# Optimization experiments

Hardware: AMD Instinct MI355X
Metric: run time of the kernel (lower is better)

The kernel has to match this reference:

```python
import jax, jax.numpy as jnp
import numpy as np

D_MODEL = 1024
D_STATE = 16
D_CONV = 4
EXPAND = 2
D_INNER = EXPAND * D_MODEL
DT_RANK = (D_MODEL + 15) // 16  # ceil(d_model/16) = 64
BATCH, SEQ = 4, 4096


def setup_inputs() -> dict:
    key = jax.random.key(0)
    ks = jax.random.split(key, 8)
    s = 0.02
    x = jax.random.normal(ks[0], (BATCH, SEQ, D_MODEL), jnp.float32)
    in_proj_w = jax.random.normal(ks[1], (2 * D_INNER, D_MODEL), jnp.float32) * s
    conv_w = jax.random.normal(ks[2], (D_INNER, D_CONV), jnp.float32) * 0.2  # depthwise kernel
    conv_b = jnp.zeros((D_INNER,), jnp.float32)
    x_proj_w = jax.random.normal(ks[3], (DT_RANK + 2 * D_STATE, D_INNER), jnp.float32) * s
    dt_proj_w = jax.random.normal(ks[4], (D_INNER, DT_RANK), jnp.float32) * s
    # standard mamba dt bias init: softplus(bias) ~ small positive dt
    dt_proj_b = jnp.log(jnp.expm1(jnp.full((D_INNER,), 1e-2, jnp.float32)))
    # S4D-real init: A = -[1..d_state] per channel
    A_log = jnp.log(jnp.tile(jnp.arange(1, D_STATE + 1, dtype=jnp.float32), (D_INNER, 1)))
    D_skip = jnp.ones((D_INNER,), jnp.float32)
    out_proj_w = jax.random.normal(ks[5], (D_MODEL, D_INNER), jnp.float32) * s
    return dict(x=x, in_proj_w=in_proj_w, conv_w=conv_w, conv_b=conv_b,
                x_proj_w=x_proj_w, dt_proj_w=dt_proj_w, dt_proj_b=dt_proj_b,
                A_log=A_log, D_skip=D_skip, out_proj_w=out_proj_w)


def _rmsnorm(x, eps=1e-6):
    # FastSimpleRMSNorm: no learned weight
    return x * jax.lax.rsqrt(jnp.mean(x * x, axis=-1, keepdims=True) + eps)


def reference(x, in_proj_w, conv_w, conv_b, x_proj_w, dt_proj_w, dt_proj_b,
              A_log, D_skip, out_proj_w):
    B_, L, _ = x.shape
    u = _rmsnorm(x)
    # in_proj -> gate z and conv branch xc, each [B, L, d_inner]
    xz = jnp.einsum('bld,ed->ble', u, in_proj_w)
    xc, z = jnp.split(xz, 2, axis=-1)
    # causal depthwise conv1d (width D_CONV) + silu
    xp = jnp.pad(xc, ((0, 0), (D_CONV - 1, 0), (0, 0)))
    conv = conv_b + sum(conv_w[:, k] * xp[:, k:k + L, :] for k in range(D_CONV))
    xc = jax.nn.silu(conv)
    # x_proj -> dt, B, C
    dbl = jnp.einsum('ble,fe->blf', xc, x_proj_w)
    dt, Bm, Cm = jnp.split(dbl, [DT_RANK, DT_RANK + D_STATE], axis=-1)
    dt = jax.nn.softplus(jnp.einsum('blr,er->ble', dt, dt_proj_w) + dt_proj_b)  # [B,L,d_inner]
    A = -jnp.exp(A_log)  # [d_inner, d_state]

    def step(h, inp):
        dt_t, B_t, C_t, x_t = inp  # [B,d_inner],[B,d_state],[B,d_state],[B,d_inner]
        dA = jnp.exp(dt_t[..., None] * A)             # [B,d_inner,d_state]
        h = h * dA + (dt_t * x_t)[..., None] * B_t[:, None, :]
        y = jnp.einsum('bes,bs->be', h, C_t)
        return h, y

    h0 = jnp.zeros((B_, D_INNER, D_STATE), xc.dtype)
    xs = (jnp.swapaxes(dt, 0, 1), jnp.swapaxes(Bm, 0, 1),
          jnp.swapaxes(Cm, 0, 1), jnp.swapaxes(xc, 0, 1))
    _, ys = jax.lax.scan(step, h0, xs)                # [L,B,d_inner]
    y = jnp.swapaxes(ys, 0, 1) + D_skip * xc
    y = y * jax.nn.silu(z)
    out = jnp.einsum('ble,de->bld', y, out_proj_w)
    return x + out
```

## Files before the change

### kernel.cpp

```cpp
#include <hip/hip_runtime.h>
#include <hip/hip_bf16.h>
#include <math.h>

typedef __hip_bfloat16 bf16;
typedef __attribute__((ext_vector_type(8))) short short8;
typedef __attribute__((ext_vector_type(4))) float f32x4;

#define BATCH_N 4
#define SEQ_N 4096
#define DMODEL 1024
#define DINNER 2048
#define DTRANK 64
#define DSTATE 16
#define NROWS (BATCH_N * SEQ_N)

__device__ __forceinline__ float b2f(bf16 v) { return __bfloat162float(v); }
__device__ __forceinline__ bf16 f2b(float v) { return __float2bfloat16(v); }

__device__ __forceinline__ void gll16(const bf16* g, bf16* l) {
    __builtin_amdgcn_global_load_lds((const __attribute__((address_space(1))) unsigned int*)g,
                                     (__attribute__((address_space(3))) unsigned int*)l,
                                     16, 0, 0);
}

#define CVT_N1 4194304
#define CVT_N2 196608
#define CVT_N3 131072
#define CVT_N4 2097152
#define CVT_TOTAL (CVT_N1 + CVT_N2 + CVT_N3 + CVT_N4)
__global__ __launch_bounds__(256) void prep_kernel(const float* __restrict__ x, bf16* __restrict__ u,
                                                   const float* __restrict__ i1, bf16* __restrict__ o1,
                                                   const float* __restrict__ i2, bf16* __restrict__ o2,
                                                   const float* __restrict__ i3, bf16* __restrict__ o3,
                                                   const float* __restrict__ i4, bf16* __restrict__ o4) {
    if (blockIdx.x < NROWS) {
        const int r = blockIdx.x;
        const int t = threadIdx.x;
        const float4 v = reinterpret_cast<const float4*>(x + (size_t)r * DMODEL)[t];
        float ss = v.x * v.x + v.y * v.y + v.z * v.z + v.w * v.w;
        #pragma unroll
        for (int o = 32; o > 0; o >>= 1) ss += __shfl_down(ss, o);
        __shared__ float red[4];
        if ((t & 63) == 0) red[t >> 6] = ss;
        __syncthreads();
        const float tot = red[0] + red[1] + red[2] + red[3];
        const float rs = rsqrtf(tot * (1.0f / DMODEL) + 1e-6f);
        union { uint2 u2; bf16 h[4]; } o4v;
        o4v.h[0] = f2b(v.x * rs); o4v.h[1] = f2b(v.y * rs);
        o4v.h[2] = f2b(v.z * rs); o4v.h[3] = f2b(v.w * rs);
        *reinterpret_cast<uint2*>(u + (size_t)r * DMODEL + t * 4) = o4v.u2;
    } else {
        int i = (blockIdx.x - NROWS) * 256 + threadIdx.x;
        if (i < CVT_N1) { o1[i] = f2b(i1[i]); }
        i -= CVT_N1;
        if (i >= 0 && i < CVT_N2) { o2[i] = f2b(i2[i]); }
        i -= CVT_N2;
        if (i >= 0 && i < CVT_N3) { o3[i] = f2b(i3[i]); }
        i -= CVT_N3;
        if (i >= 0 && i < CVT_N4) { o4[i] = f2b(i4[i]); }
    }
}

__global__ __launch_bounds__(256) void conv_silu4_kernel(const bf16* __restrict__ xcraw,
                                                         const float* __restrict__ cw,
                                                         const float* __restrict__ cb,
                                                         bf16* __restrict__ xc) {
    const int t = blockIdx.x * 256 + threadIdx.x;
    const int e = (t << 2) & (DINNER - 1);
    const int r = t >> 9;
    const int l = r & (SEQ_N - 1);
    float4 w0 = *reinterpret_cast<const float4*>(cw + (e + 0) * 4);
    float4 w1 = *reinterpret_cast<const float4*>(cw + (e + 1) * 4);
    float4 w2 = *reinterpret_cast<const float4*>(cw + (e + 2) * 4);
    float4 w3 = *reinterpret_cast<const float4*>(cw + (e + 3) * 4);
    const float4 bias = *reinterpret_cast<const float4*>(cb + e);
    float xs[4][4];
    #pragma unroll
    for (int k = 0; k < 4; ++k) {
        const int lp = l - 3 + k;
        if (lp >= 0) {
            union { uint2 u; bf16 h[4]; } tmp;
            tmp.u = *reinterpret_cast<const uint2*>(xcraw + (size_t)(r - 3 + k) * DINNER + e);
            #pragma unroll
            for (int j = 0; j < 4; ++j) xs[k][j] = b2f(tmp.h[j]);
        } else {
            #pragma unroll
            for (int j = 0; j < 4; ++j) xs[k][j] = 0.f;
        }
    }
    float acc[4];
    acc[0] = bias.x + w0.x * xs[0][0] + w0.y * xs[1][0] + w0.z * xs[2][0] + w0.w * xs[3][0];
    acc[1] = bias.y + w1.x * xs[0][1] + w1.y * xs[1][1] + w1.z * xs[2][1] + w1.w * xs[3][1];
    acc[2] = bias.z + w2.x * xs[0][2] + w2.y * xs[1][2] + w2.z * xs[2][2] + w2.w * xs[3][2];
    acc[3] = bias.w + w3.x * xs[0][3] + w3.y * xs[1][3] + w3.z * xs[2][3] + w3.w * xs[3][3];
    union { uint2 u; bf16 h[4]; } o;
    #pragma unroll
    for (int j = 0; j < 4; ++j) o.h[j] = f2b(acc[j] / (1.f + __expf(-acc[j])));
    *reinterpret_cast<uint2*>(xc + (size_t)r * DINNER + e) = o.u;
}

template <int EPI>
__global__ __launch_bounds__(256) void mfma_gemm(const bf16* __restrict__ A, int lda,
                                                 const bf16* __restrict__ B, int ldb,
                                                 void* __restrict__ Cout,
                                                 void* __restrict__ Cout2,
                                                 const float* __restrict__ aux,
                                                 int N, int K) {
    __shared__ __align__(16) bf16 sA[2][128 * 32];
    __shared__ __align__(16) bf16 sB[2][128 * 32];
    const int tid = threadIdx.x;
    const int w = tid >> 6;
    const int lane = tid & 63;
    const int quad = lane >> 4;
    const int l15 = lane & 15;
    const int m0 = blockIdx.x * 128;
    const int n0 = blockIdx.y * 128;
    const int wm = (w >> 1) * 64;
    const int wn = (w & 1) * 64;

    if constexpr (EPI == 5) {
        const int koff = blockIdx.z * K;
        A += koff;
        B += koff;
    }

    f32x4 acc[4][4];
    #pragma unroll
    for (int i = 0; i < 4; ++i)
        #pragma unroll
        for (int j = 0; j < 4; ++j)
            acc[i][j] = (f32x4){0.f, 0.f, 0.f, 0.f};

    const int sm = tid >> 2;
    const int q = (tid & 3) ^ ((sm >> 1) & 3);
    const bf16* gA0 = A + (size_t)(m0 + sm) * lda + q * 8;
    const bf16* gA1 = gA0 + (size_t)64 * lda;
    const bf16* gB0 = B + (size_t)(n0 + sm) * ldb + q * 8;
    const bf16* gB1 = gB0 + (size_t)64 * ldb;
    bf16* lA0c0 = sA[0] + w * 512;
    bf16* lA1c0 = sA[0] + 2048 + w * 512;
    bf16* lA0c1 = sA[1] + w * 512;
    bf16* lA1c1 = sA[1] + 2048 + w * 512;
    bf16* lB0c0 = sB[0] + w * 512;
    bf16* lB1c0 = sB[0] + 2048 + w * 512;
    bf16* lB0c1 = sB[1] + w * 512;
    bf16* lB1c1 = sB[1] + 2048 + w * 512;

    const int sw2 = (l15 >> 1) & 3;
    const int qx = (quad ^ sw2) * 8;

    for (int k0 = 0; k0 < K; k0 += 64) {
        gll16(gA0 + k0, lA0c0);
        gll16(gA1 + k0, lA1c0);
        gll16(gB0 + k0, lB0c0);
        gll16(gB1 + k0, lB1c0);
        gll16(gA0 + k0 + 32, lA0c1);
        gll16(gA1 + k0 + 32, lA1c1);
        gll16(gB0 + k0 + 32, lB0c1);
        gll16(gB1 + k0 + 32, lB1c1);
        __syncthreads();
        #pragma unroll
        for (int ch = 0; ch < 2; ++ch) {
            short8 af[4], bfr[4];
            #pragma unroll
            for (int f = 0; f < 4; ++f) {
                af[f]  = *reinterpret_cast<const short8*>(sA[ch] + (wm + f * 16 + l15) * 32 + qx);
                bfr[f] = *reinterpret_cast<const short8*>(sB[ch] + (wn + f * 16 + l15) * 32 + qx);
            }
            #pragma unroll
            for (int i = 0; i < 4; ++i)
                #pragma unroll
                for (int j = 0; j < 4; ++j)
                    acc[i][j] = __builtin_amdgcn_mfma_f32_16x16x32_bf16(af[i], bfr[j], acc[i][j], 0, 0, 0);
        }
        __syncthreads();
    }

    const int rbase = m0 + wm + quad * 4;
    if constexpr (EPI == 1) {
        bf16* C = (bf16*)Cout;
        #pragma unroll
        for (int i = 0; i < 4; ++i)
            #pragma unroll
            for (int r = 0; r < 4; ++r) {
                const size_t ro = (size_t)(rbase + i * 16 + r) * N;
                #pragma unroll
                for (int j = 0; j < 4; ++j) {
                    const int c = n0 + wn + j * 16 + l15;
                    float v = acc[i][j][r] + aux[c];
                    if (v < 15.f) v = __logf(1.f + __expf(v));
                    C[ro + c] = f2b(v);
                }
            }
    } else {
        float* C = (float*)Cout + (size_t)blockIdx.z * NROWS * N;
        #pragma unroll
        for (int i = 0; i < 4; ++i)
            #pragma unroll
            for (int r = 0; r < 4; ++r) {
                const size_t ro = (size_t)(rbase + i * 16 + r) * N;
                #pragma unroll
                for (int j = 0; j < 4; ++j)
                    C[ro + n0 + wn + j * 16 + l15] = acc[i][j][r];
            }
    }
    (void)Cout2;
}

template <int EPI>
__global__ __launch_bounds__(512, 2) void mfma_gemm256(const bf16* __restrict__ A, int lda,
                                                       const bf16* __restrict__ B, int ldb,
                                                       void* __restrict__ Cout,
                                                       void* __restrict__ Cout2,
                                                       const float* __restrict__ aux,
                                                       int N, int K) {
    __shared__ __align__(16) bf16 lds[4 * 16384];
    const int tid = threadIdx.x;
    const int w = tid >> 6;
    const int lane = tid & 63;
    const int quad = lane >> 4;
    const int l15 = lane & 15;
    const int nwg = gridDim.x;
    const int wg = (blockIdx.x & 7) * (nwg >> 3) + (blockIdx.x >> 3);
    const int m0 = (wg & 63) * 256;
    const int n0 = (wg >> 6) * 256;
    const int wr = w >> 2;
    const int wc = w & 3;

    f32x4 acc[8][4];
    #pragma unroll
    for (int i = 0; i < 8; ++i)
        #pragma unroll
        for (int j = 0; j < 4; ++j) acc[i][j] = (f32x4){0.f, 0.f, 0.f, 0.f};

    const int srow = tid >> 2;
    const int su = ((tid & 3) ^ ((tid >> 3) & 3)) * 8;
    const bf16* gA0 = A + (size_t)(m0 + srow) * lda + su;
    const bf16* gA1 = gA0 + (size_t)128 * lda;
    const bf16* gB0 = B + (size_t)(n0 + srow) * ldb + su;
    const bf16* gB1 = gB0 + (size_t)128 * ldb;
    const int wofs = w * 512;

    const int qx = (quad ^ ((l15 >> 1) & 3)) * 8;
    const int arow = wr * 128 + l15;
    const int brow = wc * 64 + l15;
    const int nk = K >> 5;

    auto STAGE = [&](int s) {
        bf16* base = lds + (s & 3) * 16384;
        const size_t ko = (size_t)s * 32;
        gll16(gA0 + ko, base + wofs);
        gll16(gA1 + ko, base + 4096 + wofs);
        gll16(gB0 + ko, base + 8192 + wofs);
        gll16(gB1 + ko, base + 12288 + wofs);
    };
    STAGE(0); STAGE(1); STAGE(2);

    for (int t = 0; t < nk; ++t) {
        const int rem = nk - 1 - t;
        if (rem >= 2)      asm volatile("s_waitcnt vmcnt(8)" ::: "memory");
        else if (rem == 1) asm volatile("s_waitcnt vmcnt(4)" ::: "memory");
        else               asm volatile("s_waitcnt vmcnt(0)" ::: "memory");
        __builtin_amdgcn_s_barrier();
        asm volatile("" ::: "memory");
        const bf16* bufA = lds + (t & 3) * 16384;
        const bf16* bufB = bufA + 8192;
        short8 af[8], bfr[4];
        #pragma unroll
        for (int i = 0; i < 8; ++i)
            af[i] = *reinterpret_cast<const short8*>(bufA + (arow + i * 16) * 32 + qx);
        #pragma unroll
        for (int j = 0; j < 4; ++j)
            bfr[j] = *reinterpret_cast<const short8*>(bufB + (brow + j * 16) * 32 + qx);
        if (t + 3 < nk) STAGE(t + 3);
        #pragma unroll
        for (int i = 0; i < 8; ++i)
            #pragma unroll
            for (int j = 0; j < 4; ++j)
                acc[i][j] = __builtin_amdgcn_mfma_f32_16x16x32_bf16(af[i], bfr[j], acc[i][j], 0, 0, 0);
    }

    const int rbase = m0 + wr * 128 + quad * 4;
    if constexpr (EPI == 2) {
        float* C = (float*)Cout;
        #pragma unroll
        for (int i = 0; i < 8; ++i)
            #pragma unroll
            for (int r = 0; r < 4; ++r) {
                const size_t ro = (size_t)(rbase + i * 16 + r) * N;
                #pragma unroll
                for (int j = 0; j < 4; ++j) {
                    const int c = n0 + wc * 64 + j * 16 + l15;
                    C[ro + c] = acc[i][j][r] + aux[ro + c];
                }
            }
    } else {
        bf16* C = (bf16*)((n0 < 2048) ? Cout : Cout2);
        const int cb = (n0 & 2047) + wc * 64;
        #pragma unroll
        for (int i = 0; i < 8; ++i)
            #pragma unroll
            for (int r = 0; r < 4; ++r) {
                const size_t ro = (size_t)(rbase + i * 16 + r) * 2048;
                #pragma unroll
                for (int j = 0; j < 4; ++j)
                    C[ro + cb + j * 16 + l15] = f2b(acc[i][j][r]);
            }
    }
    (void)aux;
}

__global__ __launch_bounds__(256) void combine_xproj(const float* __restrict__ p0,
                                                     const float* __restrict__ p1,
                                                     bf16* __restrict__ dtr,
                                                     float* __restrict__ bcbuf) {
    const int idx = blockIdx.x * 256 + threadIdx.x;
    const int c = idx & 127;
    const int row = idx >> 7;
    const float v = p0[idx] + p1[idx];
    if (c < 64) dtr[(size_t)row * 64 + c] = f2b(v);
    else if (c < 96) bcbuf[(size_t)row * 32 + (c - 64)] = v;
}

__device__ __forceinline__ bool pow_ok(const float* a) {
    bool ok = true;
    #pragma unroll
    for (int s = 1; s < 16; ++s) {
        const float t = a[0] * (s + 1);
        ok = ok && (fabsf(a[s] - t) <= 1e-4f * fabsf(t) + 1e-6f);
    }
    return ok;
}

template <int NC>
__global__ __launch_bounds__(256) void scan_passA(const bf16* __restrict__ dt,
                                                  const bf16* __restrict__ xc,
                                                  const float* __restrict__ bcbuf,
                                                  const float* __restrict__ A_log,
                                                  float* __restrict__ hend,
                                                  float* __restrict__ sumdt) {
    constexpr int LC = SEQ_N / NC;
    __shared__ __align__(16) float sbc[LC * 32];
    const int e = blockIdx.x * 256 + threadIdx.x;
    const int c = blockIdx.y;
    const int b = blockIdx.z;
    const size_t rbase = (size_t)b * SEQ_N + (size_t)c * LC;
    #pragma unroll
    for (int idx = threadIdx.x; idx < LC * 8; idx += 256)
        reinterpret_cast<float4*>(sbc)[idx] =
            reinterpret_cast<const float4*>(bcbuf + rbase * 32)[idx];
    float a[16], h[16];
    #pragma unroll
    for (int s = 0; s < 16; ++s) {
        a[s] = -__expf(A_log[e * 16 + s]);
        h[s] = 0.f;
    }
    const bool pw = pow_ok(a);
    float sd = 0.f;
    __syncthreads();
    for (int i = 0; i < LC; ++i) {
        const size_t row = rbase + i;
        const float dtv = b2f(dt[row * DINNER + e]);
        const float xv = b2f(xc[row * DINNER + e]);
        const float cdx = dtv * xv;
        const float4* bp = reinterpret_cast<const float4*>(sbc + i * 32);
        float Bv[16];
        *reinterpret_cast<float4*>(&Bv[0])  = bp[0];
        *reinterpret_cast<float4*>(&Bv[4])  = bp[1];
        *reinterpret_cast<float4*>(&Bv[8])  = bp[2];
        *reinterpret_cast<float4*>(&Bv[12]) = bp[3];
        sd += dtv;
        if (pw) {
            const float e1 = __expf(dtv * a[0]);
            float dAp = 1.f;
            #pragma unroll
            for (int s = 0; s < 16; ++s) {
                dAp *= e1;
                h[s] = fmaf(h[s], dAp, cdx * Bv[s]);
            }
        } else {
            #pragma unroll
            for (int s = 0; s < 16; ++s) {
                const float dA = __expf(dtv * a[s]);
                h[s] = fmaf(h[s], dA, cdx * Bv[s]);
            }
        }
    }
    const size_t o = ((size_t)b * NC + c) * DINNER + e;
    #pragma unroll
    for (int s = 0; s < 16; s += 4) {
        float4 v = {h[s], h[s + 1], h[s + 2], h[s + 3]};
        *reinterpret_cast<float4*>(hend + o * 16 + s) = v;
    }
    sumdt[o] = sd;
}

template <int NC>
__global__ __launch_bounds__(256) void scan_passB(float* hstate,
                                                  const float* __restrict__ sumdt,
                                                  const float* __restrict__ A_log) {
    const int g = blockIdx.x * 256 + threadIdx.x;
    const int s = g & 15;
    const int e = (g >> 4) & (DINNER - 1);
    const int b = g >> 15;
    const float a = -__expf(A_log[e * 16 + s]);
    float H = 0.f;
    for (int c = 0; c < NC; ++c) {
        const size_t o = ((size_t)b * NC + c) * DINNER + e;
        const float he = hstate[o * 16 + s];
        const float sd = sumdt[o];
        hstate[o * 16 + s] = H;
        H = fmaf(H, __expf(a * sd), he);
    }
}

template <int NC>
__global__ __launch_bounds__(256) void scan_passC(const bf16* dt,
                                                  const bf16* __restrict__ xc,
                                                  const bf16* __restrict__ z,
                                                  const float* __restrict__ bcbuf,
                                                  const float* __restrict__ A_log,
                                                  const float* __restrict__ D_skip,
                                                  const float* __restrict__ hinit,
                                                  bf16* y) {
    constexpr int LC = SEQ_N / NC;
    __shared__ __align__(16) float sbc[LC * 32];
    const int e = blockIdx.x * 256 + threadIdx.x;
    const int c = blockIdx.y;
    const int b = blockIdx.z;
    const size_t rbase = (size_t)b * SEQ_N + (size_t)c * LC;
    #pragma unroll
    for (int idx = threadIdx.x; idx < LC * 8; idx += 256)
        reinterpret_cast<float4*>(sbc)[idx] =
            reinterpret_cast<const float4*>(bcbuf + rbase * 32)[idx];
    float a[16], h[16];
    #pragma unroll
    for (int s = 0; s < 16; ++s) a[s] = -__expf(A_log[e * 16 + s]);
    const bool pw = pow_ok(a);
    const float dsk = D_skip[e];
    const size_t o = ((size_t)b * NC + c) * DINNER + e;
    #pragma unroll
    for (int s = 0; s < 16; s += 4) {
        float4 v = *reinterpret_cast<const float4*>(hinit + o * 16 + s);
        h[s] = v.x; h[s + 1] = v.y; h[s + 2] = v.z; h[s + 3] = v.w;
    }
    __syncthreads();
    for (int i = 0; i < LC; ++i) {
        const size_t row = rbase + i;
        const float dtv = b2f(dt[row * DINNER + e]);
        const float xv = b2f(xc[row * DINNER + e]);
        const float zv = b2f(z[row * DINNER + e]);
        const float cdx = dtv * xv;
        const float4* bp = reinterpret_cast<const float4*>(sbc + i * 32);
        float Bv[16], Cv[16];
        *reinterpret_cast<float4*>(&Bv[0])  = bp[0];
        *reinterpret_cast<float4*>(&Bv[4])  = bp[1];
        *reinterpret_cast<float4*>(&Bv[8])  = bp[2];
        *reinterpret_cast<float4*>(&Bv[12]) = bp[3];
        *reinterpret_cast<float4*>(&Cv[0])  = bp[4];
        *reinterpret_cast<float4*>(&Cv[4])  = bp[5];
        *reinterpret_cast<float4*>(&Cv[8])  = bp[6];
        *reinterpret_cast<float4*>(&Cv[12]) = bp[7];
        float yv = 0.f;
        if (pw) {
            const float e1 = __expf(dtv * a[0]);
            float dAp = 1.f;
            #pragma unroll
            for (int s = 0; s < 16; ++s) {
                dAp *= e1;
                h[s] = fmaf(h[s], dAp, cdx * Bv[s]);
                yv = fmaf(h[s], Cv[s], yv);
            }
        } else {
            #pragma unroll
            for (int s = 0; s < 16; ++s) {
                const float dA = __expf(dtv * a[s]);
                h[s] = fmaf(h[s], dA, cdx * Bv[s]);
                yv = fmaf(h[s], Cv[s], yv);
            }
        }
        const float g = (yv + dsk * xv) * (zv / (1.f + __expf(-zv)));
        y[row * DINNER + e] = f2b(g);
    }
}

extern "C" void kernel_launch(void* const* d_in, const int* in_sizes, int n_in,
                              void* d_out, int out_size, void* d_ws, size_t ws_size,
                              hipStream_t stream) {
    const float* x         = (const float*)d_in[0];
    const float* in_proj_w = (const float*)d_in[1];
    const float* conv_w    = (const float*)d_in[2];
    const float* conv_b    = (const float*)d_in[3];
    const float* x_proj_w  = (const float*)d_in[4];
    const float* dt_proj_w = (const float*)d_in[5];
    const float* dt_proj_b = (const float*)d_in[6];
    const float* A_log     = (const float*)d_in[7];
    const float* D_skip    = (const float*)d_in[8];
    const float* out_proj_w= (const float*)d_in[9];
    float* out = (float*)d_out;

    char* ws = (char*)d_ws;
    bf16*  xcraw = (bf16*)(ws + 0);
    bf16*  xc    = (bf16*)(ws + 67108864);
    bf16*  dtr   = (bf16*)(ws + 134217728);
    float* bcbuf = (float*)(ws + 136314880);
    bf16*  w_in  = (bf16*)(ws + 140509184);
    bf16*  w_xp  = (bf16*)(ws + 148897792);
    bf16*  w_dt  = (bf16*)(ws + 149422080);
    bf16*  w_out = (bf16*)(ws + 149684224);
    float* hend  = (float*)(ws + 153878528);
    bf16*  u     = xc;
    bf16*  dtb   = xcraw;
    bf16*  yb    = dtb;
    bf16*  zbuf  = (bf16*)d_out;
    float* xp_p0 = hend;
    float* xp_p1 = hend + (size_t)NROWS * 128;

    const bool big = (ws_size >= 189530112ULL);
    float* sumdt = (float*)(ws + (big ? 187432960 : 170655744));

    prep_kernel<<<NROWS + CVT_TOTAL / 256, 256, 0, stream>>>(
        x, u, in_proj_w, w_in, x_proj_w, w_xp, dt_proj_w, w_dt, out_proj_w, w_out);
    mfma_gemm256<3><<<dim3((NROWS / 256) * (4096 / 256)), 512, 0, stream>>>(
        u, DMODEL, w_in, DMODEL, xcraw, zbuf, nullptr, 4096, DMODEL);
    conv_silu4_kernel<<<(NROWS * DINNER) / 1024, 256, 0, stream>>>(xcraw, conv_w, conv_b, xc);
    mfma_gemm<5><<<dim3(NROWS / 128, 1, 2), 256, 0, stream>>>(
        xc, DINNER, w_xp, DINNER, xp_p0, nullptr, nullptr, 128, DINNER / 2);
    combine_xproj<<<(NROWS * 128) / 256, 256, 0, stream>>>(xp_p0, xp_p1, dtr, bcbuf);
    mfma_gemm<1><<<dim3(NROWS / 128, DINNER / 128), 256, 0, stream>>>(
        dtr, DTRANK, w_dt, DTRANK, dtb, nullptr, dt_proj_b, DINNER, DTRANK);
    if (big) {
        scan_passA<64><<<dim3(DINNER / 256, 64, BATCH_N), 256, 0, stream>>>(
            dtb, xc, bcbuf, A_log, hend, sumdt);
        scan_passB<64><<<(BATCH_N * DINNER * DSTATE) / 256, 256, 0, stream>>>(hend, sumdt, A_log);
        scan_passC<64><<<dim3(DINNER / 256, 64, BATCH_N), 256, 0, stream>>>(
            dtb, xc, zbuf, bcbuf, A_log, D_skip, hend, yb);
    } else {
        scan_passA<32><<<dim3(DINNER / 256, 32, BATCH_N), 256, 0, stream>>>(
            dtb, xc, bcbuf, A_log, hend, sumdt);
        scan_passB<32><<<(BATCH_N * DINNER * DSTATE) / 256, 256, 0, stream>>>(hend, sumdt, A_log);
        scan_passC<32><<<dim3(DINNER / 256, 32, BATCH_N), 256, 0, stream>>>(
            dtb, xc, zbuf, bcbuf, A_log, D_skip, hend, yb);
    }
    mfma_gemm256<2><<<dim3((NROWS / 256) * (DMODEL / 256)), 512, 0, stream>>>(
        yb, DINNER, w_out, DINNER, out, nullptr, x, DMODEL, DINNER);
    (void)in_sizes; (void)n_in; (void)out_size;
}
```

Before: 657.1 us.

## Restructure 256x256 GEMM into double-buffered K=64 ping-pong with interleaved loads

The big MFMA GEMM moves from a 4-stage ring of K=32 tiles to a 2-buffer scheme with K=64 tiles. Each tile is consumed in four phases, and each phase issues a slice of the next tile's global-to-LDS loads, then runs its MFMAs at raised wave priority between barriers. The intent is to overlap memory traffic with matrix math more finely, in the style of HipKittens ping-pong scheduling. It adds more barriers per iteration, changes the LDS swizzle and staging mapping, and keeps the same LDS footprint.

```diff
diff --git a/kernel.cpp b/kernel.cpp
--- a/kernel.cpp
+++ b/kernel.cpp
@@ -214,7 +214,7 @@
                                                        void* __restrict__ Cout2,
                                                        const float* __restrict__ aux,
                                                        int N, int K) {
-    __shared__ __align__(16) bf16 lds[4 * 16384];
+    __shared__ __align__(16) bf16 lds[2 * 32768];
     const int tid = threadIdx.x;
     const int w = tid >> 6;
     const int lane = tid & 63;
@@ -233,51 +233,68 @@
         #pragma unroll
         for (int j = 0; j < 4; ++j) acc[i][j] = (f32x4){0.f, 0.f, 0.f, 0.f};
 
-    const int srow = tid >> 2;
-    const int su = ((tid & 3) ^ ((tid >> 3) & 3)) * 8;
-    const bf16* gA0 = A + (size_t)(m0 + srow) * lda + su;
+    const int sr = (w << 4) | (lane >> 2);
+    const int su0 = ((lane & 3) ^ ((sr >> 1) & 3)) * 8;
+    const bf16* gA0 = A + (size_t)(m0 + sr) * lda + su0;
     const bf16* gA1 = gA0 + (size_t)128 * lda;
-    const bf16* gB0 = B + (size_t)(n0 + srow) * ldb + su;
+    const bf16* gB0 = B + (size_t)(n0 + sr) * ldb + su0;
     const bf16* gB1 = gB0 + (size_t)128 * ldb;
-    const int wofs = w * 512;
 
     const int qx = (quad ^ ((l15 >> 1) & 3)) * 8;
     const int arow = wr * 128 + l15;
     const int brow = wc * 64 + l15;
-    const int nk = K >> 5;
-
-    auto STAGE = [&](int s) {
-        bf16* base = lds + (s & 3) * 16384;
-        const size_t ko = (size_t)s * 32;
-        gll16(gA0 + ko, base + wofs);
-        gll16(gA1 + ko, base + 4096 + wofs);
-        gll16(gB0 + ko, base + 8192 + wofs);
-        gll16(gB1 + ko, base + 12288 + wofs);
+    const int nk = K >> 6;
+
+    auto STAGE = [&](int t, int pc) {
+        bf16* base = lds + (t & 1) * 32768 + ((pc & 1) << 14) + ((pc >> 1) << 13) + (w << 9);
+        const size_t ko = (size_t)t * 64 + (size_t)(pc >> 1) * 32;
+        const bf16* g0 = (pc & 1) ? gB0 : gA0;
+        const bf16* g1 = (pc & 1) ? gB1 : gA1;
+        gll16(g0 + ko, base);
+        gll16(g1 + ko, base + 4096);
     };
-    STAGE(0); STAGE(1); STAGE(2);
+    STAGE(0, 0); STAGE(0, 1); STAGE(0, 2); STAGE(0, 3);
+    asm volatile("s_waitcnt vmcnt(4)" ::: "memory");
+    __builtin_amdgcn_s_barrier();
 
     for (int t = 0; t < nk; ++t) {
-        const int rem = nk - 1 - t;
-        if (rem >= 2)      asm volatile("s_waitcnt vmcnt(8)" ::: "memory");
-        else if (rem == 1) asm volatile("s_waitcnt vmcnt(4)" ::: "memory");
-        else               asm volatile("s_waitcnt vmcnt(0)" ::: "memory");
-        __builtin_amdgcn_s_barrier();
-        asm volatile("" ::: "memory");
-        const bf16* bufA = lds + (t & 3) * 16384;
-        const bf16* bufB = bufA + 8192;
-        short8 af[8], bfr[4];
-        #pragma unroll
-        for (int i = 0; i < 8; ++i)
-            af[i] = *reinterpret_cast<const short8*>(bufA + (arow + i * 16) * 32 + qx);
-        #pragma unroll
-        for (int j = 0; j < 4; ++j)
-            bfr[j] = *reinterpret_cast<const short8*>(bufB + (brow + j * 16) * 32 + qx);
-        if (t + 3 < nk) STAGE(t + 3);
-        #pragma unroll
-        for (int i = 0; i < 8; ++i)
-            #pragma unroll
-            for (int j = 0; j < 4; ++j)
-                acc[i][j] = __builtin_amdgcn_mfma_f32_16x16x32_bf16(af[i], bfr[j], acc[i][j], 0, 0, 0);
+        const bf16* bufA = lds + (t & 1) * 32768;
+        const bf16* bufB = bufA + 16384;
+        short8 bfr[4];
+        #pragma unroll
+        for (int p = 0; p < 4; ++p) {
+            const int kk = p >> 1;
+            const int ih = p & 1;
+            short8 af[4];
+            #pragma unroll
+            for (int i = 0; i < 4; ++i)
+                af[i] = *reinterpret_cast<const short8*>(
+                    bufA + kk * 8192 + (arow + (ih * 4 + i) * 16) * 32 + qx);
+            if (ih == 0) {
+                #pragma unroll
+                for (int j = 0; j < 4; ++j)
+                    bfr[j] = *reinterpret_cast<const short8*>(
+                        bufB + kk * 8192 + (brow + j * 16) * 32 + qx);
+            }
+            if (t + 1 < nk) STAGE(t + 1, p);
+            __builtin_amdgcn_s_barrier();
+            asm volatile("s_waitcnt lgkmcnt(0)" ::: "memory");
+            __builtin_amdgcn_sched_barrier(0);
+            __builtin_amdgcn_s_setprio(1);
+            #pragma unroll
+            for (int i = 0; i < 4; ++i)
+                #pragma unroll
+                for (int j = 0; j < 4; ++j)
+                    acc[ih * 4 + i][j] =
+                        __builtin_amdgcn_mfma_f32_16x16x32_bf16(af[i], bfr[j], acc[ih * 4 + i][j], 0, 0, 0);
+            __builtin_amdgcn_s_setprio(0);
+            __builtin_amdgcn_sched_barrier(0);
+            if (ih == 1) {
+                if (t + 1 < nk) asm volatile("s_waitcnt vmcnt(4)" ::: "memory");
+                else            asm volatile("s_waitcnt vmcnt(0)" ::: "memory");
+            }
+            __builtin_amdgcn_s_barrier();
+        }
     }
 
     const int rbase = m0 + wr * 128 + quad * 4;
```

Result: no change. 659.8 us (+0.4%).

## Double-buffer GEMM LDS fragment reads to overlap with MFMA compute

Applied to the files above, without the earlier changes.

Restructures the GEMM main loop so the LDS fragment reads for the next k-step are issued before the MFMAs of the current step, using two register fragment sets in a ping-pong and a loop unrolled by two. This hides LDS read latency behind matrix-core work. It costs extra VGPRs for the second fragment set, which may lower occupancy or cause spills. The second STEP in each iteration also runs unguarded and assumes nk is even, and the vmcnt waits are retuned for the new ordering.

```diff
diff --git a/kernel.cpp b/kernel.cpp
--- a/kernel.cpp
+++ b/kernel.cpp
@@ -254,30 +254,49 @@
         gll16(gB0 + ko, base + 8192 + wofs);
         gll16(gB1 + ko, base + 12288 + wofs);
     };
-    STAGE(0); STAGE(1); STAGE(2);
-
-    for (int t = 0; t < nk; ++t) {
-        const int rem = nk - 1 - t;
-        if (rem >= 2)      asm volatile("s_waitcnt vmcnt(8)" ::: "memory");
-        else if (rem == 1) asm volatile("s_waitcnt vmcnt(4)" ::: "memory");
-        else               asm volatile("s_waitcnt vmcnt(0)" ::: "memory");
+    auto READF = [&](int s, short8* af, short8* bfr) {
+        const bf16* bufA = lds + (s & 3) * 16384;
+        const bf16* bufB = bufA + 8192;
+        #pragma unroll
+        for (int i = 0; i < 8; ++i)
+            af[i] = *reinterpret_cast<const short8*>(bufA + (arow + i * 16) * 32 + qx);
+        #pragma unroll
+        for (int j = 0; j < 4; ++j)
+            bfr[j] = *reinterpret_cast<const short8*>(bufB + (brow + j * 16) * 32 + qx);
+    };
+    auto MM = [&](short8* af, short8* bfr) {
+        #pragma unroll
+        for (int i = 0; i < 8; ++i)
+            #pragma unroll
+            for (int j = 0; j < 4; ++j)
+                acc[i][j] = __builtin_amdgcn_mfma_f32_16x16x32_bf16(af[i], bfr[j], acc[i][j], 0, 0, 0);
+    };
+
+    short8 afA[8], bfA[4], afB[8], bfB[4];
+
+    STAGE(0);
+    if (1 < nk) STAGE(1);
+    if (2 < nk) STAGE(2);
+    asm volatile("s_waitcnt vmcnt(8)" ::: "memory");
+    __builtin_amdgcn_s_barrier();
+    asm volatile("" ::: "memory");
+    READF(0, afA, bfA);
+
+    auto STEP = [&](int t, short8* afc, short8* bfc, short8* afn, short8* bfn) {
+        if (t + 1 < nk) {
+            if (t + 2 < nk) asm volatile("s_waitcnt vmcnt(4)" ::: "memory");
+            else            asm volatile("s_waitcnt vmcnt(0)" ::: "memory");
+        }
         __builtin_amdgcn_s_barrier();
         asm volatile("" ::: "memory");
-        const bf16* bufA = lds + (t & 3) * 16384;
-        const bf16* bufB = bufA + 8192;
-        short8 af[8], bfr[4];
-        #pragma unroll
-        for (int i = 0; i < 8; ++i)
-            af[i] = *reinterpret_cast<const short8*>(bufA + (arow + i * 16) * 32 + qx);
-        #pragma unroll
-        for (int j = 0; j < 4; ++j)
-            bfr[j] = *reinterpret_cast<const short8*>(bufB + (brow + j * 16) * 32 + qx);
         if (t + 3 < nk) STAGE(t + 3);
-        #pragma unroll
-        for (int i = 0; i < 8; ++i)
-            #pragma unroll
-            for (int j = 0; j < 4; ++j)
-                acc[i][j] = __builtin_amdgcn_mfma_f32_16x16x32_bf16(af[i], bfr[j], acc[i][j], 0, 0, 0);
+        if (t + 1 < nk) READF(t + 1, afn, bfn);
+        MM(afc, bfc);
+    };
+
+    for (int t = 0; t < nk; t += 2) {
+        STEP(t, afA, bfA, afB, bfB);
+        STEP(t + 1, afB, bfB, afA, bfA);
     }
 
     const int rbase = m0 + wr * 128 + quad * 4;
```

Measured after the change: 657.5 us. No clear change (+0.1%).
